# Optimization experiments

Measured on AMD Instinct MI355X. Metric: run time of the kernel, lower is better.

The kernel has to match this reference:

```python
import jax, jax.numpy as jnp
import numpy as np

K = 4096          # infeatures
N = 4096          # outfeatures (already multiple of 32, padding = 0)
M = 8192
GROUPS = 32       # K / group_size, group_size = 128


def setup_inputs() -> dict:
    key = jax.random.key(0)
    k1, k2, k3, k4, k5, k6 = jax.random.split(key, 6)
    x = jax.random.normal(k1, (M, K), dtype=jnp.float16)
    # packed INT4 weights: 8 nibbles per int32 along the K dimension
    q_weight = jax.random.randint(k2, (K // 8, N), 0, 2**31 - 1, dtype=jnp.int32)
    # packed 4-bit group scales: 8 nibbles per int32 along the N dimension
    q_scale = jax.random.randint(k3, (GROUPS, N // 8), 0, 2**31 - 1, dtype=jnp.int32)
    q_scale_max = (jax.random.uniform(k4, (GROUPS,), dtype=jnp.float32) + 0.5).astype(jnp.float16)
    q_invperm = jax.random.permutation(k5, K).astype(jnp.int32)
    bias = (jax.random.normal(k6, (N,), dtype=jnp.float32) * 0.02).astype(jnp.float16)
    return {"x": x, "q_weight": q_weight, "q_scale": q_scale,
            "q_scale_max": q_scale_max, "q_invperm": q_invperm, "bias": bias}


def _unpack_nibbles(packed, axis):
    # packed int32 -> 8 unsigned 4-bit values expanded along `axis`
    shifts = jnp.arange(8, dtype=jnp.int32) * 4
    shp = [1] * (packed.ndim + 1)
    shp[axis + 1] = 8
    vals = (jnp.expand_dims(packed, axis + 1) >> shifts.reshape(shp)) & 0xF
    out_shape = list(packed.shape)
    out_shape[axis] *= 8
    return vals.reshape(out_shape)


def reference(x, q_weight, q_scale, q_scale_max, q_invperm, bias):
    # --- group-wise INT4 dequantization (EXL2-style scale math) ---
    # per-group/column scale: ((s4 + 1)^2) * (q_scale_max / 256)
    s4 = _unpack_nibbles(q_scale, axis=1).astype(jnp.float16)          # [G, N]
    smax = (q_scale_max.astype(jnp.float32) / 256.0).astype(jnp.float16)
    scale = (s4 + 1.0) * (s4 + 1.0) * smax[:, None]                    # [G, N]
    w4 = _unpack_nibbles(q_weight, axis=0)                              # [K, N], 0..15
    group_size = w4.shape[0] // scale.shape[0]
    scale_rows = jnp.repeat(scale, group_size, axis=0)                  # [K, N]
    W = (w4.astype(jnp.float16) - jnp.float16(8.0)) * scale_rows        # [K, N] fp16
    # --- row permutation fused with GEMM: x is gathered by q_perm ---
    q_perm = jnp.argsort(q_invperm)                                     # [K]
    xp = jnp.take(x.astype(jnp.float16), q_perm, axis=1)                # [M, K]
    out = jnp.matmul(xp, W, preferred_element_type=jnp.float32).astype(jnp.float16)
    out = out + bias
    return out.astype(x.dtype)
```

## Files before the change

kernel.cpp:

```cpp
#include <hip/hip_runtime.h>
#include <stdint.h>

#define K_DIM 4096
#define N_DIM 4096
#define M_DIM 8192

#define BM 256
#define BN 256
#define BK 64
#define NT (K_DIM / BK)

typedef __bf16 bf16x8 __attribute__((ext_vector_type(8)));
typedef _Float16 f16x8 __attribute__((ext_vector_type(8)));
typedef unsigned short u16x8 __attribute__((ext_vector_type(8)));
typedef float floatx4 __attribute__((ext_vector_type(4)));

__device__ __attribute__((aligned(256))) unsigned short g_Bt[(size_t)N_DIM * K_DIM];
__device__ __attribute__((aligned(256))) unsigned short g_X [(size_t)M_DIM * K_DIM];
__device__ int g_flags[2];
__device__ int g_counts[4];

__device__ __forceinline__ void global_to_lds16(const void* g, void* l) {
    __builtin_amdgcn_global_load_lds(
        (const __attribute__((address_space(1))) uint32_t*)g,
        (__attribute__((address_space(3))) uint32_t*)l,
        16, 0, 0);
}

#define LDS_FENCE() asm volatile("" ::: "memory")
#define BARRIER() do { LDS_FENCE(); __builtin_amdgcn_s_barrier(); LDS_FENCE(); } while (0)

__global__ void probe_kernel(const void* xraw, const int* candA, const int* candB) {
    __shared__ int s[4];
    if (threadIdx.x < 4) s[threadIdx.x] = 0;
    __syncthreads();
    const uint16_t* xw = (const uint16_t*)xraw;
    const int gidx = blockIdx.x * 256 + threadIdx.x;
    int insane = 0, small = 0;
    {
        uint16_t a = (uint16_t)(xw[2 * gidx] & 0x7FFF);
        if (a >= 0x4300) insane++;
        if (a > 0 && a < 0x3000) small++;
    }
    int badA = 0, badB = 0;
    if (gidx < 4096) {
        if ((unsigned)candA[gidx] >= 4096u) badA++;
        if ((unsigned)candB[gidx] >= 4096u) badB++;
    }
    atomicAdd(&s[0], insane); atomicAdd(&s[1], small);
    atomicAdd(&s[2], badA);   atomicAdd(&s[3], badB);
    __syncthreads();
    if (threadIdx.x < 4 && s[threadIdx.x] != 0) atomicAdd(&g_counts[threadIdx.x], s[threadIdx.x]);
}

__global__ void finalize_kernel() {
    int insane = g_counts[0], small = g_counts[1];
    int badA = g_counts[2], badB = g_counts[3];
    int mode = 0;
    if (insane > 32) mode = 1;
    else if (small > 100) mode = 2;
    g_flags[0] = mode;
    g_flags[1] = (badA > 0 && badB == 0) ? 1 : 0;
    g_counts[0] = g_counts[1] = g_counts[2] = g_counts[3] = 0;
}

__global__ void __launch_bounds__(256) convert_x_kernel(const void* xraw) {
    if (g_flags[0] != 1) return;
    const size_t nchunk = (size_t)M_DIM * K_DIM / 8;
    const float* xf = (const float*)xraw;
    for (size_t c = (size_t)blockIdx.x * 256 + threadIdx.x; c < nchunk;
         c += (size_t)gridDim.x * 256) {
        size_t base = c * 8;
        float4 v0 = *(const float4*)(xf + base);
        float4 v1 = *(const float4*)(xf + base + 4);
        u16x8 o;
        _Float16 h;
        h = (_Float16)v0.x; o[0] = __builtin_bit_cast(unsigned short, h);
        h = (_Float16)v0.y; o[1] = __builtin_bit_cast(unsigned short, h);
        h = (_Float16)v0.z; o[2] = __builtin_bit_cast(unsigned short, h);
        h = (_Float16)v0.w; o[3] = __builtin_bit_cast(unsigned short, h);
        h = (_Float16)v1.x; o[4] = __builtin_bit_cast(unsigned short, h);
        h = (_Float16)v1.y; o[5] = __builtin_bit_cast(unsigned short, h);
        h = (_Float16)v1.z; o[6] = __builtin_bit_cast(unsigned short, h);
        h = (_Float16)v1.w; o[7] = __builtin_bit_cast(unsigned short, h);
        *(u16x8*)(g_X + base) = o;
    }
}

__global__ void __launch_bounds__(256) dequant_perm_kernel(
    const int* __restrict__ q_weight,
    const int* __restrict__ q_scale,
    const void* __restrict__ qsm_raw,
    const int* __restrict__ candA, const int* __restrict__ candB)
{
    __shared__ __attribute__((aligned(16))) unsigned short lds[16 * 136];

    const int mode = g_flags[0];
    const int* q_invperm = g_flags[1] ? candB : candA;

    const int n_l  = threadIdx.x & 15;
    const int jp_l = threadIdx.x >> 4;
    const int n  = blockIdx.x * 16 + n_l;
    const int j0 = (blockIdx.y * 16 + jp_l) << 3;

    int4 ip0 = *(const int4*)(q_invperm + j0);
    int4 ip1 = *(const int4*)(q_invperm + j0 + 4);
    int ks[8] = {ip0.x, ip0.y, ip0.z, ip0.w, ip1.x, ip1.y, ip1.z, ip1.w};

    const int nshift = (n & 7) << 2;
    const int scol = n >> 3;

    u16x8 ov;
#pragma unroll
    for (int u = 0; u < 8; ++u) {
        int k = ks[u] & (K_DIM - 1);
        int w4 = (q_weight[(size_t)(k >> 3) * N_DIM + n] >> ((k & 7) << 2)) & 0xF;
        int g = k >> 7;
        int s4 = (q_scale[g * (N_DIM / 8) + scol] >> nshift) & 0xF;
        float smax;
        if (mode == 1)      smax = ((const float*)qsm_raw)[g];
        else if (mode == 2) smax = (float)((const _Float16*)qsm_raw)[g];
        else                smax = (float)((const __bf16*)qsm_raw)[g];
        float sp1 = (float)(s4 + 1);
        float w = (float)(w4 - 8) * (sp1 * sp1 * smax * (1.0f / 256.0f));
        if (mode != 0) { _Float16 h = (_Float16)w; ov[u] = __builtin_bit_cast(unsigned short, h); }
        else           { __bf16   b = (__bf16)w;   ov[u] = __builtin_bit_cast(unsigned short, b); }
    }
    *(u16x8*)&lds[n_l * 136 + jp_l * 8] = ov;
    __syncthreads();

    const int row = threadIdx.x >> 4;
    const int c16 = threadIdx.x & 15;
    u16x8 t = *(const u16x8*)&lds[row * 136 + c16 * 8];
    *(u16x8*)(g_Bt + (size_t)(blockIdx.x * 16 + row) * K_DIM
              + (size_t)blockIdx.y * 128 + c16 * 8) = t;
}

template <bool F16>
__global__ void __launch_bounds__(512, 2) gemm_bt_kernel(
    const void* __restrict__ xraw,
    const void* __restrict__ bias_candA, const void* __restrict__ bias_candB,
    void* __restrict__ outraw)
{
    const int mode = g_flags[0];
    if (F16 != (mode != 0)) return;

    __shared__ __attribute__((aligned(128))) unsigned short sm[4 * 256 * 64];
    const int ASZ = 256 * 64;
    const int SB  = 2 * ASZ;

    const void* bias_raw = g_flags[1] ? bias_candA : bias_candB;
    const unsigned short* __restrict__ Xp =
        (mode == 1) ? g_X : (const unsigned short*)xraw;
    const unsigned short* __restrict__ Bt = g_Bt;

    const int tid  = threadIdx.x;
    const int wave = tid >> 6;
    const int lane = tid & 63;

    const int orig = blockIdx.y * 16 + blockIdx.x;
    const int swz  = (orig & 7) * 64 + (orig >> 3);
    const int bn0  = (swz & 15) * BN;
    const int bm0  = (swz >> 4) * BM;

    const int lrow8 = lane >> 3;
    const int ksw   = ((lane & 7) ^ lrow8) << 3;
    const size_t aoff = (size_t)(bm0 + wave * 8 + lrow8) * K_DIM + ksw;
    const size_t boff = (size_t)(bn0 + wave * 8 + lrow8) * K_DIM + ksw;
    const int ldsw = (wave * 8) * 64;

    const int w_m16 = (wave >> 2) << 4;
    const int w_n16 = (wave & 3) << 4;
    const int frow  = lane & 15;
    const int fk    = (lane >> 4) << 3;
    const int ksw8  = (lane & 7) << 3;

    floatx4 acc[8][4] = {};
    u16x8 a[4][2], b[4][2];

#define STAGE_A(bufbase, h, c, ktt) \
    global_to_lds16(Xp + aoff + (size_t)((h) * 128 + (c) * 64) * K_DIM + (ktt), \
                    &sm[(bufbase) + ((h) * 128 + (c) * 64) * 64 + ldsw])
#define STAGE_B(bufbase, h, c, ktt) \
    global_to_lds16(Bt + boff + (size_t)((h) * 128 + (c) * 64) * K_DIM + (ktt), \
                    &sm[SB + (bufbase) + ((h) * 128 + (c) * 64) * 64 + ldsw])

#define MFMA_PH(ibase, jbase) do { \
    __builtin_amdgcn_s_setprio(1); \
    _Pragma("unroll") \
    for (int ii = 0; ii < 4; ++ii) \
        _Pragma("unroll") \
        for (int jj = 0; jj < 2; ++jj) \
            _Pragma("unroll") \
            for (int kh = 0; kh < 2; ++kh) { \
                if constexpr (F16) \
                    acc[(ibase) + ii][(jbase) + jj] = __builtin_amdgcn_mfma_f32_16x16x32_f16( \
                        __builtin_bit_cast(f16x8, a[ii][kh]), \
                        __builtin_bit_cast(f16x8, b[(jbase) + jj][kh]), \
                        acc[(ibase) + ii][(jbase) + jj], 0, 0, 0); \
                else \
                    acc[(ibase) + ii][(jbase) + jj] = __builtin_amdgcn_mfma_f32_16x16x32_bf16( \
                        __builtin_bit_cast(bf16x8, a[ii][kh]), \
                        __builtin_bit_cast(bf16x8, b[(jbase) + jj][kh]), \
                        acc[(ibase) + ii][(jbase) + jj], 0, 0, 0); \
            } \
    __builtin_amdgcn_s_setprio(0); \
} while (0)

    STAGE_A(0, 0, 0, 0); STAGE_A(0, 0, 1, 0);
    STAGE_B(0, 0, 0, 0); STAGE_B(0, 0, 1, 0);
    STAGE_B(0, 1, 0, 0); STAGE_B(0, 1, 1, 0);
    STAGE_A(0, 1, 0, 0); STAGE_A(0, 1, 1, 0);
    asm volatile("s_waitcnt vmcnt(4)" ::: "memory");
    BARRIER();

    int cur = 0;
#pragma unroll 1
    for (int t = 0; t < NT; ++t) {
        const int nxt = cur ^ 1;
        const int curA = cur * ASZ;
        const int curB = cur * ASZ;
        const int nbA = nxt * ASZ;
        const int nbB = nxt * ASZ;
        const bool st = (t + 1 < NT);
        const int kt1 = (t + 1) * BK;

#pragma unroll
        for (int ii = 0; ii < 4; ++ii)
#pragma unroll
            for (int kh = 0; kh < 2; ++kh)
                a[ii][kh] = *(const u16x8*)&sm[curA + (ii * 32 + w_m16 + frow) * 64
                                              + ((kh * 32 + fk) ^ ksw8)];
#pragma unroll
        for (int j = 0; j < 2; ++j)
#pragma unroll
            for (int kh = 0; kh < 2; ++kh)
                b[j][kh] = *(const u16x8*)&sm[SB + curB + (j * 64 + w_n16 + frow) * 64
                                              + ((kh * 32 + fk) ^ ksw8)];
        if (st) { STAGE_A(nbA, 0, 0, kt1); STAGE_A(nbA, 0, 1, kt1); }
        if (st) asm volatile("s_waitcnt vmcnt(4) lgkmcnt(0)" ::: "memory");
        else    asm volatile("s_waitcnt vmcnt(2) lgkmcnt(0)" ::: "memory");
        BARRIER();
        MFMA_PH(0, 0);

#pragma unroll
        for (int j = 2; j < 4; ++j)
#pragma unroll
            for (int kh = 0; kh < 2; ++kh)
                b[j][kh] = *(const u16x8*)&sm[SB + curB + (j * 64 + w_n16 + frow) * 64
                                              + ((kh * 32 + fk) ^ ksw8)];
        if (st) { STAGE_B(nbB, 0, 0, kt1); STAGE_B(nbB, 0, 1, kt1); }
        if (st) asm volatile("s_waitcnt vmcnt(4) lgkmcnt(0)" ::: "memory");
        else    asm volatile("s_waitcnt vmcnt(0) lgkmcnt(0)" ::: "memory");
        BARRIER();
        MFMA_PH(0, 2);

#pragma unroll
        for (int ii = 0; ii < 4; ++ii)
#pragma unroll
            for (int kh = 0; kh < 2; ++kh)
                a[ii][kh] = *(const u16x8*)&sm[curA + ((ii + 4) * 32 + w_m16 + frow) * 64
                                               + ((kh * 32 + fk) ^ ksw8)];
        if (st) { STAGE_B(nbB, 1, 0, kt1); STAGE_B(nbB, 1, 1, kt1); }
        asm volatile("s_waitcnt lgkmcnt(0)" ::: "memory");
        BARRIER();
        MFMA_PH(4, 2);

        if (st) {
            STAGE_A(nbA, 1, 0, kt1); STAGE_A(nbA, 1, 1, kt1);
            asm volatile("s_waitcnt vmcnt(4)" ::: "memory");
        }
        BARRIER();
        MFMA_PH(4, 0);

        cur = nxt;
    }

    const int ccol = lane & 15;
    const int crow = (lane >> 4) << 2;
#pragma unroll
    for (int j = 0; j < 4; ++j) {
        const int col = bn0 + j * 64 + w_n16 + ccol;
        float bv;
        if (mode == 1)      bv = ((const float*)bias_raw)[col];
        else if (mode == 2) bv = (float)((const _Float16*)bias_raw)[col];
        else                bv = (float)((const __bf16*)bias_raw)[col];
#pragma unroll
        for (int i = 0; i < 8; ++i) {
            const int row = bm0 + i * 32 + w_m16 + crow;
#pragma unroll
            for (int r = 0; r < 4; ++r) {
                float v = acc[i][j][r] + bv;
                size_t idx = (size_t)(row + r) * N_DIM + col;
                if (mode == 1)      ((float*)outraw)[idx] = v;
                else if (mode == 2) ((_Float16*)outraw)[idx] = (_Float16)v;
                else                ((__bf16*)outraw)[idx] = (__bf16)v;
            }
        }
    }
#undef STAGE_A
#undef STAGE_B
#undef MFMA_PH
}

extern "C" void kernel_launch(void* const* d_in, const int* in_sizes, int n_in,
                              void* d_out, int out_size, void* d_ws, size_t ws_size,
                              hipStream_t stream) {
    int idx_x = 0, idx_qw = 1, idx_qs = 2, idx_qsm = 3, idx_a = -1, idx_b = -1;
    for (int i = 0; i < n_in; ++i) {
        switch (in_sizes[i]) {
            case 33554432: idx_x = i; break;
            case 2097152:  idx_qw = i; break;
            case 16384:    idx_qs = i; break;
            case 32:       idx_qsm = i; break;
            case 4096:     (idx_a < 0 ? idx_a : idx_b) = i; break;
            default: break;
        }
    }
    if (idx_a < 0) idx_a = 4;
    if (idx_b < 0) idx_b = 5;

    const void* xraw  = d_in[idx_x];
    const int*  qw    = (const int*)d_in[idx_qw];
    const int*  qs    = (const int*)d_in[idx_qs];
    const void* qsm   = d_in[idx_qsm];
    const int*  candA = (const int*)d_in[idx_a];
    const int*  candB = (const int*)d_in[idx_b];

    probe_kernel<<<32, 256, 0, stream>>>(xraw, candA, candB);
    finalize_kernel<<<1, 1, 0, stream>>>();
    convert_x_kernel<<<2048, 256, 0, stream>>>(xraw);
    dim3 dqg(N_DIM / 16, (K_DIM / 8) / 16);
    dequant_perm_kernel<<<dqg, 256, 0, stream>>>(qw, qs, qsm, candA, candB);
    dim3 grid(N_DIM / BN, M_DIM / BM);
    gemm_bt_kernel<true ><<<grid, 512, 0, stream>>>(xraw, d_in[idx_a], d_in[idx_b], d_out);
    gemm_bt_kernel<false><<<grid, 512, 0, stream>>>(xraw, d_in[idx_a], d_in[idx_b], d_out);
}
```

Baseline: 479.9 us.

## Restructure GEMM main loop into two-tile unrolled quadrant schedule with new warp mapping

Rewrites the GEMM main loop to process two K tiles per iteration, splitting the 256x256 block tile into four 128x128 quadrants per K step. Each quadrant's LDS reads overlap asynchronous global-to-LDS staging of future tiles. It also changes the wave-to-fragment mapping so each wave owns contiguous 64x32 sub-tiles per quadrant instead of strided rows. The goal is a steadier overlap of memory loads with MFMA work, at the cost of more barriers per iteration and tighter vmcnt bookkeeping.

```diff
diff --git a/kernel.cpp b/kernel.cpp
--- a/kernel.cpp
+++ b/kernel.cpp
@@ -145,9 +145,7 @@
     const int mode = g_flags[0];
     if (F16 != (mode != 0)) return;
 
-    __shared__ __attribute__((aligned(128))) unsigned short sm[4 * 256 * 64];
-    const int ASZ = 256 * 64;
-    const int SB  = 2 * ASZ;
+    __shared__ __attribute__((aligned(128))) unsigned short sm[65536];
 
     const void* bias_raw = g_flags[1] ? bias_candA : bias_candB;
     const unsigned short* __restrict__ Xp =
@@ -165,132 +163,125 @@
 
     const int lrow8 = lane >> 3;
     const int ksw   = ((lane & 7) ^ lrow8) << 3;
-    const size_t aoff = (size_t)(bm0 + wave * 8 + lrow8) * K_DIM + ksw;
-    const size_t boff = (size_t)(bn0 + wave * 8 + lrow8) * K_DIM + ksw;
-    const int ldsw = (wave * 8) * 64;
-
-    const int w_m16 = (wave >> 2) << 4;
-    const int w_n16 = (wave & 3) << 4;
-    const int frow  = lane & 15;
-    const int fk    = (lane >> 4) << 3;
-    const int ksw8  = (lane & 7) << 3;
-
-    floatx4 acc[8][4] = {};
-    u16x8 a[4][2], b[4][2];
-
-#define STAGE_A(bufbase, h, c, ktt) \
-    global_to_lds16(Xp + aoff + (size_t)((h) * 128 + (c) * 64) * K_DIM + (ktt), \
-                    &sm[(bufbase) + ((h) * 128 + (c) * 64) * 64 + ldsw])
-#define STAGE_B(bufbase, h, c, ktt) \
-    global_to_lds16(Bt + boff + (size_t)((h) * 128 + (c) * 64) * K_DIM + (ktt), \
-                    &sm[SB + (bufbase) + ((h) * 128 + (c) * 64) * 64 + ldsw])
-
-#define MFMA_PH(ibase, jbase) do { \
+    const unsigned short* Xs = Xp + (size_t)(bm0 + wave * 8 + lrow8) * K_DIM + ksw;
+    const unsigned short* Bs = Bt + (size_t)(bn0 + wave * 8 + lrow8) * K_DIM + ksw;
+    const int sdst = wave * 512 + lane * 8;
+
+    const int wm   = wave >> 2;
+    const int wn   = wave & 3;
+    const int frow = lane & 15;
+    const int fk   = (lane >> 4) << 3;
+    const int kx   = (lane & 7) << 3;
+    const int arow = (wm * 64 + frow) * 64;
+    const int brow = (wn * 32 + frow) * 64;
+
+    floatx4 acc[2][2][4][2] = {};
+    u16x8 a[4][2];
+    u16x8 b[2][2][2];
+
+#define VM4() asm volatile("s_waitcnt vmcnt(4)" ::: "memory")
+#define VM6() asm volatile("s_waitcnt vmcnt(6)" ::: "memory")
+#define VM0() asm volatile("s_waitcnt vmcnt(0)" ::: "memory")
+#define LG0() asm volatile("s_waitcnt lgkmcnt(0)" ::: "memory")
+
+#define ST_A(d, h, kt) do { \
+    _Pragma("unroll") for (int r = 0; r < 2; ++r) \
+        global_to_lds16(Xs + (size_t)((h) * 128 + r * 64) * K_DIM + (kt), \
+                        &sm[(d) * 16384 + (h) * 8192 + r * 4096 + sdst]); } while (0)
+#define ST_B(d, h, kt) do { \
+    _Pragma("unroll") for (int r = 0; r < 2; ++r) \
+        global_to_lds16(Bs + (size_t)((h) * 128 + r * 64) * K_DIM + (kt), \
+                        &sm[32768 + (d) * 16384 + (h) * 8192 + r * 4096 + sdst]); } while (0)
+#define RD_A(d, mh) do { \
+    _Pragma("unroll") for (int fi = 0; fi < 4; ++fi) \
+    _Pragma("unroll") for (int k2 = 0; k2 < 2; ++k2) \
+        a[fi][k2] = *(const u16x8*)&sm[(d) * 16384 + (mh) * 8192 + arow + fi * 1024 \
+                                       + ((k2 * 32 + fk) ^ kx)]; } while (0)
+#define RD_B(d, nh) do { \
+    _Pragma("unroll") for (int fj = 0; fj < 2; ++fj) \
+    _Pragma("unroll") for (int k2 = 0; k2 < 2; ++k2) \
+        b[nh][fj][k2] = *(const u16x8*)&sm[32768 + (d) * 16384 + (nh) * 8192 + brow + fj * 1024 \
+                                           + ((k2 * 32 + fk) ^ kx)]; } while (0)
+#define MM16(mh, nh) do { \
     __builtin_amdgcn_s_setprio(1); \
-    _Pragma("unroll") \
-    for (int ii = 0; ii < 4; ++ii) \
-        _Pragma("unroll") \
-        for (int jj = 0; jj < 2; ++jj) \
-            _Pragma("unroll") \
-            for (int kh = 0; kh < 2; ++kh) { \
-                if constexpr (F16) \
-                    acc[(ibase) + ii][(jbase) + jj] = __builtin_amdgcn_mfma_f32_16x16x32_f16( \
-                        __builtin_bit_cast(f16x8, a[ii][kh]), \
-                        __builtin_bit_cast(f16x8, b[(jbase) + jj][kh]), \
-                        acc[(ibase) + ii][(jbase) + jj], 0, 0, 0); \
-                else \
-                    acc[(ibase) + ii][(jbase) + jj] = __builtin_amdgcn_mfma_f32_16x16x32_bf16( \
-                        __builtin_bit_cast(bf16x8, a[ii][kh]), \
-                        __builtin_bit_cast(bf16x8, b[(jbase) + jj][kh]), \
-                        acc[(ibase) + ii][(jbase) + jj], 0, 0, 0); \
-            } \
-    __builtin_amdgcn_s_setprio(0); \
-} while (0)
-
-    STAGE_A(0, 0, 0, 0); STAGE_A(0, 0, 1, 0);
-    STAGE_B(0, 0, 0, 0); STAGE_B(0, 0, 1, 0);
-    STAGE_B(0, 1, 0, 0); STAGE_B(0, 1, 1, 0);
-    STAGE_A(0, 1, 0, 0); STAGE_A(0, 1, 1, 0);
-    asm volatile("s_waitcnt vmcnt(4)" ::: "memory");
+    _Pragma("unroll") for (int fi = 0; fi < 4; ++fi) \
+    _Pragma("unroll") for (int fj = 0; fj < 2; ++fj) \
+    _Pragma("unroll") for (int k2 = 0; k2 < 2; ++k2) { \
+        if constexpr (F16) \
+            acc[mh][nh][fi][fj] = __builtin_amdgcn_mfma_f32_16x16x32_f16( \
+                __builtin_bit_cast(f16x8, a[fi][k2]), __builtin_bit_cast(f16x8, b[nh][fj][k2]), \
+                acc[mh][nh][fi][fj], 0, 0, 0); \
+        else \
+            acc[mh][nh][fi][fj] = __builtin_amdgcn_mfma_f32_16x16x32_bf16( \
+                __builtin_bit_cast(bf16x8, a[fi][k2]), __builtin_bit_cast(bf16x8, b[nh][fj][k2]), \
+                acc[mh][nh][fi][fj], 0, 0, 0); \
+    } \
+    __builtin_amdgcn_s_setprio(0); } while (0)
+
+    ST_A(0, 0, 0); ST_A(0, 1, 0); ST_B(0, 0, 0); ST_B(0, 1, 0);
+    ST_A(1, 0, BK); ST_A(1, 1, BK); ST_B(1, 0, BK);
+    VM6();
     BARRIER();
 
-    int cur = 0;
 #pragma unroll 1
-    for (int t = 0; t < NT; ++t) {
-        const int nxt = cur ^ 1;
-        const int curA = cur * ASZ;
-        const int curB = cur * ASZ;
-        const int nbA = nxt * ASZ;
-        const int nbB = nxt * ASZ;
-        const bool st = (t + 1 < NT);
-        const int kt1 = (t + 1) * BK;
-
-#pragma unroll
-        for (int ii = 0; ii < 4; ++ii)
-#pragma unroll
-            for (int kh = 0; kh < 2; ++kh)
-                a[ii][kh] = *(const u16x8*)&sm[curA + (ii * 32 + w_m16 + frow) * 64
-                                              + ((kh * 32 + fk) ^ ksw8)];
-#pragma unroll
-        for (int j = 0; j < 2; ++j)
-#pragma unroll
-            for (int kh = 0; kh < 2; ++kh)
-                b[j][kh] = *(const u16x8*)&sm[SB + curB + (j * 64 + w_n16 + frow) * 64
-                                              + ((kh * 32 + fk) ^ ksw8)];
-        if (st) { STAGE_A(nbA, 0, 0, kt1); STAGE_A(nbA, 0, 1, kt1); }
-        if (st) asm volatile("s_waitcnt vmcnt(4) lgkmcnt(0)" ::: "memory");
-        else    asm volatile("s_waitcnt vmcnt(2) lgkmcnt(0)" ::: "memory");
+    for (int J = 0; J < NT / 2; ++J) {
+        const int kQ  = 2 * J * BK + BK;
+        const int kP2 = 2 * J * BK + 2 * BK;
+        const int kQ2 = 2 * J * BK + 3 * BK;
+        const bool stg = (J + 1 < NT / 2);
+
+        RD_A(0, 0); RD_B(0, 0);
+        ST_B(1, 1, kQ);
+        BARRIER(); LG0(); MM16(0, 0); BARRIER();
+
+        RD_B(0, 1);
+        if (stg) ST_A(0, 0, kP2);
+        BARRIER(); LG0(); MM16(0, 1); BARRIER();
+
+        RD_A(0, 1);
+        BARRIER(); LG0(); MM16(1, 0); BARRIER();
+
+        if (stg) ST_A(0, 1, kP2);
+        BARRIER(); LG0(); MM16(1, 1);
+        if (stg) VM4(); else VM0();
         BARRIER();
-        MFMA_PH(0, 0);
-
-#pragma unroll
-        for (int j = 2; j < 4; ++j)
-#pragma unroll
-            for (int kh = 0; kh < 2; ++kh)
-                b[j][kh] = *(const u16x8*)&sm[SB + curB + (j * 64 + w_n16 + frow) * 64
-                                              + ((kh * 32 + fk) ^ ksw8)];
-        if (st) { STAGE_B(nbB, 0, 0, kt1); STAGE_B(nbB, 0, 1, kt1); }
-        if (st) asm volatile("s_waitcnt vmcnt(4) lgkmcnt(0)" ::: "memory");
-        else    asm volatile("s_waitcnt vmcnt(0) lgkmcnt(0)" ::: "memory");
+
+        RD_A(1, 0); RD_B(1, 0);
+        if (stg) { ST_B(0, 0, kP2); ST_B(0, 1, kP2); }
+        BARRIER(); LG0(); MM16(0, 0); BARRIER();
+
+        RD_B(1, 1);
+        if (stg) ST_A(1, 0, kQ2);
+        BARRIER(); LG0(); MM16(0, 1); BARRIER();
+
+        RD_A(1, 1);
+        BARRIER(); LG0(); MM16(1, 0); BARRIER();
+
+        if (stg) { ST_A(1, 1, kQ2); ST_B(1, 0, kQ2); }
+        BARRIER(); LG0(); MM16(1, 1);
+        if (stg) VM6();
         BARRIER();
-        MFMA_PH(0, 2);
-
-#pragma unroll
-        for (int ii = 0; ii < 4; ++ii)
-#pragma unroll
-            for (int kh = 0; kh < 2; ++kh)
-                a[ii][kh] = *(const u16x8*)&sm[curA + ((ii + 4) * 32 + w_m16 + frow) * 64
-                                               + ((kh * 32 + fk) ^ ksw8)];
-        if (st) { STAGE_B(nbB, 1, 0, kt1); STAGE_B(nbB, 1, 1, kt1); }
-        asm volatile("s_waitcnt lgkmcnt(0)" ::: "memory");
-        BARRIER();
-        MFMA_PH(4, 2);
-
-        if (st) {
-            STAGE_A(nbA, 1, 0, kt1); STAGE_A(nbA, 1, 1, kt1);
-            asm volatile("s_waitcnt vmcnt(4)" ::: "memory");
-        }
-        BARRIER();
-        MFMA_PH(4, 0);
-
-        cur = nxt;
     }
 
     const int ccol = lane & 15;
     const int crow = (lane >> 4) << 2;
 #pragma unroll
-    for (int j = 0; j < 4; ++j) {
-        const int col = bn0 + j * 64 + w_n16 + ccol;
+    for (int mh = 0; mh < 2; ++mh)
+#pragma unroll
+    for (int nh = 0; nh < 2; ++nh)
+#pragma unroll
+    for (int fj = 0; fj < 2; ++fj) {
+        const int col = bn0 + nh * 128 + wn * 32 + fj * 16 + ccol;
         float bv;
         if (mode == 1)      bv = ((const float*)bias_raw)[col];
         else if (mode == 2) bv = (float)((const _Float16*)bias_raw)[col];
         else                bv = (float)((const __bf16*)bias_raw)[col];
 #pragma unroll
-        for (int i = 0; i < 8; ++i) {
-            const int row = bm0 + i * 32 + w_m16 + crow;
+        for (int fi = 0; fi < 4; ++fi) {
+            const int row = bm0 + mh * 128 + wm * 64 + fi * 16 + crow;
 #pragma unroll
             for (int r = 0; r < 4; ++r) {
-                float v = acc[i][j][r] + bv;
+                float v = acc[mh][nh][fi][fj][r] + bv;
                 size_t idx = (size_t)(row + r) * N_DIM + col;
                 if (mode == 1)      ((float*)outraw)[idx] = v;
                 else if (mode == 2) ((_Float16*)outraw)[idx] = (_Float16)v;
@@ -298,9 +289,15 @@
             }
         }
     }
-#undef STAGE_A
-#undef STAGE_B
-#undef MFMA_PH
+#undef ST_A
+#undef ST_B
+#undef RD_A
+#undef RD_B
+#undef MM16
+#undef VM4
+#undef VM6
+#undef VM0
+#undef LG0
 }
 
 extern "C" void kernel_launch(void* const* d_in, const int* in_sizes, int n_in,
```

New measurement: 493.9 us. +2.9%, slower.
